# Kernel optimization log

Hardware: AMD Instinct MI355X
Metric: run time of the kernel (lower is better)

Reference implementation:

```python
import jax, jax.numpy as jnp
import numpy as np

EMB = 1024  # embedding_size in the torch module


def setup_inputs() -> dict:
    key = jax.random.key(0)
    ks = jax.random.split(key, 6)
    B, N, K = 64, 256, 4096
    y = jax.random.normal(ks[0], (B, N, 1024), dtype=jnp.float32)
    # nn.Linear weights, init normal(std=0.02), zero bias
    Wy_w = jax.random.normal(ks[1], (1024, 1024), dtype=jnp.float32) * 0.02  # [out,in]
    Wy_b = jnp.zeros((1024,), dtype=jnp.float32)
    Wz_w = jax.random.normal(ks[2], (1024, 2048), dtype=jnp.float32) * 0.02  # [out,in]
    Wz_b = jnp.zeros((1024,), dtype=jnp.float32)
    dic_z = jax.random.normal(ks[3], (K, 2048), dtype=jnp.float32)
    prior = jax.random.uniform(ks[4], (K,), dtype=jnp.float32)
    prior = prior / jnp.sum(prior)
    return {"y": y, "Wy_w": Wy_w, "Wy_b": Wy_b, "Wz_w": Wz_w, "Wz_b": Wz_b,
            "dic_z": dic_z, "prior": prior}


def reference(y, Wy_w, Wy_b, Wz_w, Wz_b, dic_z, prior):
    # h = Wy(y): [B,N,1024]; dz = Wz(dic_z): [K,1024]
    h = jnp.einsum('bni,oi->bno', y, Wy_w) + Wy_b
    dz = jnp.einsum('ki,oi->ko', dic_z, Wz_w) + Wz_b
    # attention over dictionary: [B,N,K]
    att = jax.nn.softmax(jnp.einsum('bnd,kd->bnk', h, dz) / jnp.sqrt(jnp.float32(EMB)), axis=-1)
    # z[b,n] = sum_k prior[k] * att[b,n,k] * dic_z[k]  -> [B,N,2048]
    # (avoids the [B,N,K,2048] intermediate the torch code materializes)
    z = jnp.einsum('bnk,k,ke->bne', att, prior, dic_z)
    return z
```

## Files before the change

kernel.cpp:

```cpp
#include <hip/hip_runtime.h>
#include <hip/hip_bf16.h>
#include <stdint.h>

typedef __bf16 bf16;
typedef __bf16 bf16x8 __attribute__((ext_vector_type(8)));
typedef float f32x4 __attribute__((ext_vector_type(4)));
typedef unsigned short ushort8 __attribute__((ext_vector_type(8)));

__device__ __forceinline__ void gload16(const bf16* g, char* l) {
  __builtin_amdgcn_global_load_lds(
      reinterpret_cast<const __attribute__((address_space(1))) unsigned int*>(
          reinterpret_cast<uintptr_t>(g)),
      reinterpret_cast<__attribute__((address_space(3))) unsigned int*>(
          reinterpret_cast<uintptr_t>(l)),
      16, 0, 0);
}

__global__ __launch_bounds__(256) void cast_bf16(const float* __restrict__ in,
                                                 bf16* __restrict__ out, int n8) {
  int i = blockIdx.x * blockDim.x + threadIdx.x;
  const int stride = gridDim.x * blockDim.x;
  for (; i < n8; i += stride) {
    const float4 v0 = reinterpret_cast<const float4*>(in)[i * 2];
    const float4 v1 = reinterpret_cast<const float4*>(in)[i * 2 + 1];
    bf16x8 o = { (bf16)v0.x, (bf16)v0.y, (bf16)v0.z, (bf16)v0.w,
                 (bf16)v1.x, (bf16)v1.y, (bf16)v1.z, (bf16)v1.w };
    reinterpret_cast<bf16x8*>(out)[i] = o;
  }
}

template <bool OUT_BF16, bool HAS_BIAS>
__global__ __launch_bounds__(256, 2) void gemm_occ(
    const bf16* __restrict__ A, const bf16* __restrict__ B,
    const float* __restrict__ bias, void* __restrict__ Cout,
    int M, int N, int K, float scale) {
  constexpr int BUFSZ = 32768;
  constexpr int BOFF = 16384;
  extern __shared__ char lds[];
  const int tid = threadIdx.x;
  const int lane = tid & 63, w = tid >> 6;

  const int gridN = N >> 7;
  const int nwg = gridDim.x;
  const int orig = blockIdx.x;
  int wgid;
  { const int q = nwg >> 3, r = nwg & 7, x = orig & 7, rest = orig >> 3;
    wgid = (x < r ? x * (q + 1) : r * (q + 1) + (x - r) * q) + rest; }
  const int m0 = (wgid / gridN) * 128;
  const int n0 = (wgid % gridN) * 128;

  const int srow = lane >> 3;
  const int scol = ((lane & 7) ^ srow) * 8;
  const bf16* gA = A + (size_t)(m0 + w * 32 + srow) * K + scol;
  const bf16* gB = B + (size_t)(n0 + w * 32 + srow) * K + scol;

  auto stage = [&](int t) {
    char* dst = lds + (size_t)(t & 1) * BUFSZ + (w * 32) * 128;
    const size_t kc = (size_t)t * 64;
#pragma unroll
    for (int i = 0; i < 4; ++i) {
      gload16(gA + (size_t)(i * 8) * K + kc, dst + i * 1024);
      gload16(gB + (size_t)(i * 8) * K + kc, dst + BOFF + i * 1024);
    }
  };

  const int fr = lane & 15, hi = lane >> 4;
  const int wm = w >> 1, wn = w & 1;
  const int abase = (wm * 64 + fr) * 128 + ((hi ^ (fr & 7)) << 4);
  const int bbase = BOFF + (wn * 64 + fr) * 128 + ((hi ^ (fr & 7)) << 4);

  f32x4 acc[4][4] = {};
  const int NT = K >> 6;

  stage(0);
  __syncthreads();

  for (int t = 0; t < NT; ++t) {
    const char* b = lds + (size_t)(t & 1) * BUFSZ;
    if (t + 1 < NT) stage(t + 1);
    bf16x8 a[4][2], bb[4][2];
#pragma unroll
    for (int mi = 0; mi < 4; ++mi) {
      a[mi][0] = *(const bf16x8*)(b + ((abase + mi * 2048)));
      a[mi][1] = *(const bf16x8*)(b + ((abase + mi * 2048) ^ 64));
    }
#pragma unroll
    for (int ni = 0; ni < 4; ++ni) {
      bb[ni][0] = *(const bf16x8*)(b + ((bbase + ni * 2048)));
      bb[ni][1] = *(const bf16x8*)(b + ((bbase + ni * 2048) ^ 64));
    }
#pragma unroll
    for (int mi = 0; mi < 4; ++mi)
#pragma unroll
      for (int ni = 0; ni < 4; ++ni) {
        acc[mi][ni] = __builtin_amdgcn_mfma_f32_16x16x32_bf16(a[mi][0], bb[ni][0], acc[mi][ni], 0, 0, 0);
        acc[mi][ni] = __builtin_amdgcn_mfma_f32_16x16x32_bf16(a[mi][1], bb[ni][1], acc[mi][ni], 0, 0, 0);
      }
    __syncthreads();
  }

  const int lro = hi * 4;
#pragma unroll
  for (int ni = 0; ni < 4; ++ni) {
    const int gcol = n0 + wn * 64 + ni * 16 + fr;
    float bvs = 0.f;
    if constexpr (HAS_BIAS) bvs = bias[gcol];
#pragma unroll
    for (int mi = 0; mi < 4; ++mi) {
      const int grow = m0 + wm * 64 + mi * 16 + lro;
#pragma unroll
      for (int j = 0; j < 4; ++j) {
        const float c = acc[mi][ni][j] * scale + bvs;
        if constexpr (OUT_BF16)
          ((bf16*)Cout)[(size_t)(grow + j) * N + gcol] = (bf16)c;
        else
          ((float*)Cout)[(size_t)(grow + j) * N + gcol] = c;
      }
    }
  }
}

__global__ __launch_bounds__(256) void prep_w3t(const float* __restrict__ dic,
                                                const float* __restrict__ prior,
                                                bf16* __restrict__ w3t) {
  const int KD = 4096, E = 2048;
  __shared__ bf16 t[64][72];
  const int k0 = blockIdx.x * 64, e0 = blockIdx.y * 64;
  const int tid = threadIdx.x;
  const int er = (tid & 15) * 4;
  const int kr = tid >> 4;
#pragma unroll
  for (int p = 0; p < 4; ++p) {
    const int k = kr + p * 16;
    const float pr = prior[k0 + k];
    const float4 v = *reinterpret_cast<const float4*>(dic + (size_t)(k0 + k) * E + e0 + er);
    t[er + 0][k] = (bf16)(v.x * pr);
    t[er + 1][k] = (bf16)(v.y * pr);
    t[er + 2][k] = (bf16)(v.z * pr);
    t[er + 3][k] = (bf16)(v.w * pr);
  }
  __syncthreads();
  const int e = tid >> 2, kc = (tid & 3) * 16;
  ushort8 a = *reinterpret_cast<ushort8*>(&t[e][kc]);
  ushort8 b = *reinterpret_cast<ushort8*>(&t[e][kc + 8]);
  unsigned short* dst = (unsigned short*)w3t + (size_t)(e0 + e) * KD + k0 + kc;
  *reinterpret_cast<ushort8*>(dst) = a;
  *reinterpret_cast<ushort8*>(dst + 8) = b;
}

__global__ __launch_bounds__(256) void softmax_rows(unsigned short* __restrict__ S) {
  const int K = 4096;
  unsigned short* row = S + (size_t)blockIdx.x * K;
  const int tid = threadIdx.x;
  const int lane = tid & 63, w = tid >> 6;
  __shared__ float red[8];

  ushort8 v0 = *reinterpret_cast<const ushort8*>(row + tid * 8);
  ushort8 v1 = *reinterpret_cast<const ushort8*>(row + 2048 + tid * 8);
  float x[16];
#pragma unroll
  for (int i = 0; i < 8; ++i) {
    x[i]     = __uint_as_float(((unsigned)v0[i]) << 16);
    x[8 + i] = __uint_as_float(((unsigned)v1[i]) << 16);
  }
  float mx = x[0];
#pragma unroll
  for (int i = 1; i < 16; ++i) mx = fmaxf(mx, x[i]);
#pragma unroll
  for (int o = 32; o; o >>= 1) mx = fmaxf(mx, __shfl_xor(mx, o));
  if (lane == 0) red[w] = mx;
  __syncthreads();
  mx = fmaxf(fmaxf(red[0], red[1]), fmaxf(red[2], red[3]));

  float s = 0.f;
#pragma unroll
  for (int i = 0; i < 16; ++i) { x[i] = __expf(x[i] - mx); s += x[i]; }
#pragma unroll
  for (int o = 32; o; o >>= 1) s += __shfl_xor(s, o);
  if (lane == 0) red[4 + w] = s;
  __syncthreads();
  const float inv = 1.f / (red[4] + red[5] + red[6] + red[7]);

  ushort8 o0, o1;
#pragma unroll
  for (int i = 0; i < 8; ++i) {
    bf16 b0 = (bf16)(x[i] * inv);
    bf16 b1 = (bf16)(x[8 + i] * inv);
    o0[i] = __builtin_bit_cast(unsigned short, b0);
    o1[i] = __builtin_bit_cast(unsigned short, b1);
  }
  *reinterpret_cast<ushort8*>(row + tid * 8) = o0;
  *reinterpret_cast<ushort8*>(row + 2048 + tid * 8) = o1;
}

extern "C" void kernel_launch(void* const* d_in, const int* in_sizes, int n_in,
                              void* d_out, int out_size, void* d_ws, size_t ws_size,
                              hipStream_t stream) {
  const float* y     = (const float*)d_in[0];
  const float* Wy_w  = (const float*)d_in[1];
  const float* Wy_b  = (const float*)d_in[2];
  const float* Wz_w  = (const float*)d_in[3];
  const float* Wz_b  = (const float*)d_in[4];
  const float* dic   = (const float*)d_in[5];
  const float* prior = (const float*)d_in[6];
  float* z = (float*)d_out;

  const int M = 16384, D = 1024, E = 2048, KD = 4096;
  const size_t LDSB = 65536;

  char* ws = (char*)d_ws;
  bf16* w3t  = (bf16*)(ws);
  bf16* h    = (bf16*)(ws + ((size_t)16 << 20));
  bf16* dzb  = (bf16*)(ws + ((size_t)48 << 20));
  bf16* S    = (bf16*)(ws + ((size_t)56 << 20));
  bf16* yb   = (bf16*)(ws + ((size_t)56 << 20));
  bf16* Wyb  = (bf16*)(ws + ((size_t)88 << 20));
  bf16* Wzb  = (bf16*)(ws + ((size_t)90 << 20));
  bf16* dicb = (bf16*)(ws + ((size_t)94 << 20));

  cast_bf16<<<2048, 256, 0, stream>>>(y, yb, M * D / 8);
  cast_bf16<<<512, 256, 0, stream>>>(Wy_w, Wyb, D * D / 8);
  cast_bf16<<<512, 256, 0, stream>>>(Wz_w, Wzb, D * E / 8);
  cast_bf16<<<1024, 256, 0, stream>>>(dic, dicb, KD * E / 8);
  prep_w3t<<<dim3(KD / 64, E / 64), 256, 0, stream>>>(dic, prior, w3t);
  gemm_occ<true, true><<<(M / 128) * (D / 128), 256, LDSB, stream>>>(
      yb, Wyb, Wy_b, h, M, D, D, 1.0f);
  gemm_occ<true, true><<<(KD / 128) * (D / 128), 256, LDSB, stream>>>(
      dicb, Wzb, Wz_b, dzb, KD, D, E, 1.0f);
  gemm_occ<true, false><<<(M / 128) * (KD / 128), 256, LDSB, stream>>>(
      h, dzb, nullptr, S, M, KD, D, 0.03125f);
  softmax_rows<<<M, 256, 0, stream>>>((unsigned short*)S);
  gemm_occ<false, false><<<(M / 128) * (E / 128), 256, LDSB, stream>>>(
      S, w3t, nullptr, z, M, E, KD, 1.0f);
}
```

Before: 578.8 us.

## Use 256x128 tiles with B fragments loaded directly from global into registers

```diff
diff --git a/kernel.cpp b/kernel.cpp
--- a/kernel.cpp
+++ b/kernel.cpp
@@ -30,74 +30,93 @@
 }
 
 template <bool OUT_BF16, bool HAS_BIAS>
-__global__ __launch_bounds__(256, 2) void gemm_occ(
+__global__ __launch_bounds__(256, 2) void gemm_bd(
     const bf16* __restrict__ A, const bf16* __restrict__ B,
     const float* __restrict__ bias, void* __restrict__ Cout,
     int M, int N, int K, float scale) {
   constexpr int BUFSZ = 32768;
-  constexpr int BOFF = 16384;
   extern __shared__ char lds[];
   const int tid = threadIdx.x;
   const int lane = tid & 63, w = tid >> 6;
 
-  const int gridN = N >> 7;
+  const int gridM = M >> 8;
   const int nwg = gridDim.x;
   const int orig = blockIdx.x;
   int wgid;
   { const int q = nwg >> 3, r = nwg & 7, x = orig & 7, rest = orig >> 3;
     wgid = (x < r ? x * (q + 1) : r * (q + 1) + (x - r) * q) + rest; }
-  const int m0 = (wgid / gridN) * 128;
-  const int n0 = (wgid % gridN) * 128;
+  const int m0 = (wgid % gridM) * 256;
+  const int n0 = (wgid / gridM) * 128;
 
   const int srow = lane >> 3;
   const int scol = ((lane & 7) ^ srow) * 8;
-  const bf16* gA = A + (size_t)(m0 + w * 32 + srow) * K + scol;
-  const bf16* gB = B + (size_t)(n0 + w * 32 + srow) * K + scol;
-
-  auto stage = [&](int t) {
-    char* dst = lds + (size_t)(t & 1) * BUFSZ + (w * 32) * 128;
+  const bf16* gA = A + (size_t)(m0 + w * 64 + srow) * K + scol;
+
+  auto stageA = [&](int t) {
+    char* dst = lds + (size_t)(t & 1) * BUFSZ + (w * 64) * 128;
     const size_t kc = (size_t)t * 64;
 #pragma unroll
-    for (int i = 0; i < 4; ++i) {
+    for (int i = 0; i < 8; ++i)
       gload16(gA + (size_t)(i * 8) * K + kc, dst + i * 1024);
-      gload16(gB + (size_t)(i * 8) * K + kc, dst + BOFF + i * 1024);
-    }
   };
 
   const int fr = lane & 15, hi = lane >> 4;
   const int wm = w >> 1, wn = w & 1;
-  const int abase = (wm * 64 + fr) * 128 + ((hi ^ (fr & 7)) << 4);
-  const int bbase = BOFF + (wn * 64 + fr) * 128 + ((hi ^ (fr & 7)) << 4);
-
-  f32x4 acc[4][4] = {};
+  const int abase = (wm * 128 + fr) * 128 + ((hi ^ (fr & 7)) << 4);
+
+  const bf16* gB[4];
+#pragma unroll
+  for (int ni = 0; ni < 4; ++ni)
+    gB[ni] = B + (size_t)(n0 + wn * 64 + ni * 16 + fr) * K + hi * 8;
+
+  f32x4 acc[8][4] = {};
   const int NT = K >> 6;
 
-  stage(0);
-  __syncthreads();
-
-  for (int t = 0; t < NT; ++t) {
-    const char* b = lds + (size_t)(t & 1) * BUFSZ;
-    if (t + 1 < NT) stage(t + 1);
-    bf16x8 a[4][2], bb[4][2];
-#pragma unroll
-    for (int mi = 0; mi < 4; ++mi) {
-      a[mi][0] = *(const bf16x8*)(b + ((abase + mi * 2048)));
-      a[mi][1] = *(const bf16x8*)(b + ((abase + mi * 2048) ^ 64));
-    }
-#pragma unroll
-    for (int ni = 0; ni < 4; ++ni) {
-      bb[ni][0] = *(const bf16x8*)(b + ((bbase + ni * 2048)));
-      bb[ni][1] = *(const bf16x8*)(b + ((bbase + ni * 2048) ^ 64));
-    }
-#pragma unroll
-    for (int mi = 0; mi < 4; ++mi)
-#pragma unroll
-      for (int ni = 0; ni < 4; ++ni) {
-        acc[mi][ni] = __builtin_amdgcn_mfma_f32_16x16x32_bf16(a[mi][0], bb[ni][0], acc[mi][ni], 0, 0, 0);
-        acc[mi][ni] = __builtin_amdgcn_mfma_f32_16x16x32_bf16(a[mi][1], bb[ni][1], acc[mi][ni], 0, 0, 0);
-      }
-    __syncthreads();
-  }
+  bf16x8 bA[4][2], bB[4][2];
+#define LOADB(DST, T) do {                                                     \
+    _Pragma("unroll") for (int ni = 0; ni < 4; ++ni) {                         \
+      DST[ni][0] = *(const bf16x8*)(gB[ni] + (size_t)(T) * 64);                \
+      DST[ni][1] = *(const bf16x8*)(gB[ni] + (size_t)(T) * 64 + 32);           \
+    } } while (0)
+
+  stageA(0);
+  LOADB(bA, 0);
+  __syncthreads();
+
+#define MFMA_(a0, a1, bc, accv)                                                \
+    accv = __builtin_amdgcn_mfma_f32_16x16x32_bf16(a0, bc[0], accv, 0, 0, 0); \
+    accv = __builtin_amdgcn_mfma_f32_16x16x32_bf16(a1, bc[1], accv, 0, 0, 0);
+
+#define ITER(T, BC, BN) do {                                                   \
+    const char* bp = lds + (size_t)((T) & 1) * BUFSZ;                          \
+    if ((T) + 1 < NT) { stageA((T) + 1); LOADB(BN, (T) + 1); }                 \
+    bf16x8 a[4][2];                                                            \
+    _Pragma("unroll") for (int mi = 0; mi < 4; ++mi) {                         \
+      a[mi][0] = *(const bf16x8*)(bp + (abase + mi * 2048));                   \
+      a[mi][1] = *(const bf16x8*)(bp + ((abase + mi * 2048) ^ 64));            \
+    }                                                                          \
+    _Pragma("unroll") for (int mi = 0; mi < 4; ++mi)                           \
+      _Pragma("unroll") for (int ni = 0; ni < 4; ++ni) {                       \
+        MFMA_(a[mi][0], a[mi][1], BC[ni], acc[mi][ni]);                        \
+      }                                                                        \
+    _Pragma("unroll") for (int mi = 0; mi < 4; ++mi) {                         \
+      a[mi][0] = *(const bf16x8*)(bp + (abase + (4 + mi) * 2048));             \
+      a[mi][1] = *(const bf16x8*)(bp + ((abase + (4 + mi) * 2048) ^ 64));      \
+    }                                                                          \
+    _Pragma("unroll") for (int mi = 0; mi < 4; ++mi)                           \
+      _Pragma("unroll") for (int ni = 0; ni < 4; ++ni) {                       \
+        MFMA_(a[mi][0], a[mi][1], BC[ni], acc[4 + mi][ni]);                    \
+      }                                                                        \
+    __syncthreads();                                                           \
+  } while (0)
+
+  for (int t = 0; t < NT; t += 2) {
+    ITER(t, bA, bB);
+    ITER(t + 1, bB, bA);
+  }
+#undef ITER
+#undef MFMA_
+#undef LOADB
 
   const int lro = hi * 4;
 #pragma unroll
@@ -106,8 +125,8 @@
     float bvs = 0.f;
     if constexpr (HAS_BIAS) bvs = bias[gcol];
 #pragma unroll
-    for (int mi = 0; mi < 4; ++mi) {
-      const int grow = m0 + wm * 64 + mi * 16 + lro;
+    for (int mi = 0; mi < 8; ++mi) {
+      const int grow = m0 + wm * 128 + mi * 16 + lro;
 #pragma unroll
       for (int j = 0; j < 4; ++j) {
         const float c = acc[mi][ni][j] * scale + bvs;
@@ -223,13 +242,13 @@
   cast_bf16<<<512, 256, 0, stream>>>(Wz_w, Wzb, D * E / 8);
   cast_bf16<<<1024, 256, 0, stream>>>(dic, dicb, KD * E / 8);
   prep_w3t<<<dim3(KD / 64, E / 64), 256, 0, stream>>>(dic, prior, w3t);
-  gemm_occ<true, true><<<(M / 128) * (D / 128), 256, LDSB, stream>>>(
+  gemm_bd<true, true><<<(M / 256) * (D / 128), 256, LDSB, stream>>>(
       yb, Wyb, Wy_b, h, M, D, D, 1.0f);
-  gemm_occ<true, true><<<(KD / 128) * (D / 128), 256, LDSB, stream>>>(
+  gemm_bd<true, true><<<(KD / 256) * (D / 128), 256, LDSB, stream>>>(
       dicb, Wzb, Wz_b, dzb, KD, D, E, 1.0f);
-  gemm_occ<true, false><<<(M / 128) * (KD / 128), 256, LDSB, stream>>>(
+  gemm_bd<true, false><<<(M / 256) * (KD / 128), 256, LDSB, stream>>>(
       h, dzb, nullptr, S, M, KD, D, 0.03125f);
   softmax_rows<<<M, 256, 0, stream>>>((unsigned short*)S);
-  gemm_occ<false, false><<<(M / 128) * (E / 128), 256, LDSB, stream>>>(
+  gemm_bd<false, false><<<(M / 256) * (E / 128), 256, LDSB, stream>>>(
       S, w3t, nullptr, z, M, E, KD, 1.0f);
 }
```

New measurement: 803.0 us. 38.7% more time.

## Switch GEMMs to 32x32x16 MFMA with fragment-ordered LDS layout; fuse dic cast

Applied to the files above, without the earlier changes.

```diff
diff --git a/kernel.cpp b/kernel.cpp
--- a/kernel.cpp
+++ b/kernel.cpp
@@ -3,8 +3,9 @@
 #include <stdint.h>
 
 typedef __bf16 bf16;
+typedef __bf16 bf16x4 __attribute__((ext_vector_type(4)));
 typedef __bf16 bf16x8 __attribute__((ext_vector_type(8)));
-typedef float f32x4 __attribute__((ext_vector_type(4)));
+typedef float f32x16 __attribute__((ext_vector_type(16)));
 typedef unsigned short ushort8 __attribute__((ext_vector_type(8)));
 
 __device__ __forceinline__ void gload16(const bf16* g, char* l) {
@@ -30,7 +31,7 @@
 }
 
 template <bool OUT_BF16, bool HAS_BIAS>
-__global__ __launch_bounds__(256, 2) void gemm_occ(
+__global__ __launch_bounds__(256, 2) void gemm32(
     const bf16* __restrict__ A, const bf16* __restrict__ B,
     const float* __restrict__ bias, void* __restrict__ Cout,
     int M, int N, int K, float scale) {
@@ -49,27 +50,25 @@
   const int m0 = (wgid / gridN) * 128;
   const int n0 = (wgid % gridN) * 128;
 
-  const int srow = lane >> 3;
-  const int scol = ((lane & 7) ^ srow) * 8;
-  const bf16* gA = A + (size_t)(m0 + w * 32 + srow) * K + scol;
-  const bf16* gB = B + (size_t)(n0 + w * 32 + srow) * K + scol;
+  const int frow = lane & 31;
+  const int fkh  = lane >> 5;
+  const bf16* gA = A + (size_t)(m0 + w * 32 + frow) * K + fkh * 8;
+  const bf16* gB = B + (size_t)(n0 + w * 32 + frow) * K + fkh * 8;
 
   auto stage = [&](int t) {
-    char* dst = lds + (size_t)(t & 1) * BUFSZ + (w * 32) * 128;
+    char* dst = lds + (size_t)(t & 1) * BUFSZ + w * 4096;
     const size_t kc = (size_t)t * 64;
 #pragma unroll
-    for (int i = 0; i < 4; ++i) {
-      gload16(gA + (size_t)(i * 8) * K + kc, dst + i * 1024);
-      gload16(gB + (size_t)(i * 8) * K + kc, dst + BOFF + i * 1024);
+    for (int ks = 0; ks < 4; ++ks) {
+      gload16(gA + kc + ks * 16, dst + ks * 1024);
+      gload16(gB + kc + ks * 16, dst + BOFF + ks * 1024);
     }
   };
 
-  const int fr = lane & 15, hi = lane >> 4;
   const int wm = w >> 1, wn = w & 1;
-  const int abase = (wm * 64 + fr) * 128 + ((hi ^ (fr & 7)) << 4);
-  const int bbase = BOFF + (wn * 64 + fr) * 128 + ((hi ^ (fr & 7)) << 4);
-
-  f32x4 acc[4][4] = {};
+  const int lofs = lane * 16;
+
+  f32x16 acc[2][2] = {};
   const int NT = K >> 6;
 
   stage(0);
@@ -78,50 +77,52 @@
   for (int t = 0; t < NT; ++t) {
     const char* b = lds + (size_t)(t & 1) * BUFSZ;
     if (t + 1 < NT) stage(t + 1);
-    bf16x8 a[4][2], bb[4][2];
-#pragma unroll
-    for (int mi = 0; mi < 4; ++mi) {
-      a[mi][0] = *(const bf16x8*)(b + ((abase + mi * 2048)));
-      a[mi][1] = *(const bf16x8*)(b + ((abase + mi * 2048) ^ 64));
-    }
-#pragma unroll
-    for (int ni = 0; ni < 4; ++ni) {
-      bb[ni][0] = *(const bf16x8*)(b + ((bbase + ni * 2048)));
-      bb[ni][1] = *(const bf16x8*)(b + ((bbase + ni * 2048) ^ 64));
-    }
-#pragma unroll
-    for (int mi = 0; mi < 4; ++mi)
-#pragma unroll
-      for (int ni = 0; ni < 4; ++ni) {
-        acc[mi][ni] = __builtin_amdgcn_mfma_f32_16x16x32_bf16(a[mi][0], bb[ni][0], acc[mi][ni], 0, 0, 0);
-        acc[mi][ni] = __builtin_amdgcn_mfma_f32_16x16x32_bf16(a[mi][1], bb[ni][1], acc[mi][ni], 0, 0, 0);
-      }
+    bf16x8 a[2][4], bb[2][4];
+#pragma unroll
+    for (int ti = 0; ti < 2; ++ti)
+#pragma unroll
+      for (int ks = 0; ks < 4; ++ks)
+        a[ti][ks] = *(const bf16x8*)(b + ((wm * 2 + ti) * 4 + ks) * 1024 + lofs);
+#pragma unroll
+    for (int ni = 0; ni < 2; ++ni)
+#pragma unroll
+      for (int ks = 0; ks < 4; ++ks)
+        bb[ni][ks] = *(const bf16x8*)(b + BOFF + ((wn * 2 + ni) * 4 + ks) * 1024 + lofs);
+#pragma unroll
+    for (int ks = 0; ks < 4; ++ks)
+#pragma unroll
+      for (int ti = 0; ti < 2; ++ti)
+#pragma unroll
+        for (int ni = 0; ni < 2; ++ni)
+          acc[ti][ni] = __builtin_amdgcn_mfma_f32_32x32x16_bf16(
+              a[ti][ks], bb[ni][ks], acc[ti][ni], 0, 0, 0);
     __syncthreads();
   }
 
-  const int lro = hi * 4;
-#pragma unroll
-  for (int ni = 0; ni < 4; ++ni) {
-    const int gcol = n0 + wn * 64 + ni * 16 + fr;
+#pragma unroll
+  for (int ni = 0; ni < 2; ++ni) {
+    const int gcol = n0 + wn * 64 + ni * 32 + frow;
     float bvs = 0.f;
     if constexpr (HAS_BIAS) bvs = bias[gcol];
 #pragma unroll
-    for (int mi = 0; mi < 4; ++mi) {
-      const int grow = m0 + wm * 64 + mi * 16 + lro;
-#pragma unroll
-      for (int j = 0; j < 4; ++j) {
-        const float c = acc[mi][ni][j] * scale + bvs;
+    for (int ti = 0; ti < 2; ++ti) {
+      const int rowb = m0 + wm * 64 + ti * 32 + 4 * fkh;
+#pragma unroll
+      for (int r = 0; r < 16; ++r) {
+        const int grow = rowb + (r & 3) + 8 * (r >> 2);
+        const float c = acc[ti][ni][r] * scale + bvs;
         if constexpr (OUT_BF16)
-          ((bf16*)Cout)[(size_t)(grow + j) * N + gcol] = (bf16)c;
+          ((bf16*)Cout)[(size_t)grow * N + gcol] = (bf16)c;
         else
-          ((float*)Cout)[(size_t)(grow + j) * N + gcol] = c;
+          ((float*)Cout)[(size_t)grow * N + gcol] = c;
       }
     }
   }
 }
 
-__global__ __launch_bounds__(256) void prep_w3t(const float* __restrict__ dic,
+__global__ __launch_bounds__(256) void prep_dic(const float* __restrict__ dic,
                                                 const float* __restrict__ prior,
+                                                bf16* __restrict__ dicb,
                                                 bf16* __restrict__ w3t) {
   const int KD = 4096, E = 2048;
   __shared__ bf16 t[64][72];
@@ -134,6 +135,8 @@
     const int k = kr + p * 16;
     const float pr = prior[k0 + k];
     const float4 v = *reinterpret_cast<const float4*>(dic + (size_t)(k0 + k) * E + e0 + er);
+    bf16x4 db = { (bf16)v.x, (bf16)v.y, (bf16)v.z, (bf16)v.w };
+    *reinterpret_cast<bf16x4*>(dicb + (size_t)(k0 + k) * E + e0 + er) = db;
     t[er + 0][k] = (bf16)(v.x * pr);
     t[er + 1][k] = (bf16)(v.y * pr);
     t[er + 2][k] = (bf16)(v.z * pr);
@@ -221,15 +224,14 @@
   cast_bf16<<<2048, 256, 0, stream>>>(y, yb, M * D / 8);
   cast_bf16<<<512, 256, 0, stream>>>(Wy_w, Wyb, D * D / 8);
   cast_bf16<<<512, 256, 0, stream>>>(Wz_w, Wzb, D * E / 8);
-  cast_bf16<<<1024, 256, 0, stream>>>(dic, dicb, KD * E / 8);
-  prep_w3t<<<dim3(KD / 64, E / 64), 256, 0, stream>>>(dic, prior, w3t);
-  gemm_occ<true, true><<<(M / 128) * (D / 128), 256, LDSB, stream>>>(
+  prep_dic<<<dim3(KD / 64, E / 64), 256, 0, stream>>>(dic, prior, dicb, w3t);
+  gemm32<true, true><<<(M / 128) * (D / 128), 256, LDSB, stream>>>(
       yb, Wyb, Wy_b, h, M, D, D, 1.0f);
-  gemm_occ<true, true><<<(KD / 128) * (D / 128), 256, LDSB, stream>>>(
+  gemm32<true, true><<<(KD / 128) * (D / 128), 256, LDSB, stream>>>(
       dicb, Wzb, Wz_b, dzb, KD, D, E, 1.0f);
-  gemm_occ<true, false><<<(M / 128) * (KD / 128), 256, LDSB, stream>>>(
+  gemm32<true, false><<<(M / 128) * (KD / 128), 256, LDSB, stream>>>(
       h, dzb, nullptr, S, M, KD, D, 0.03125f);
   softmax_rows<<<M, 256, 0, stream>>>((unsigned short*)S);
-  gemm_occ<false, false><<<(M / 128) * (E / 128), 256, LDSB, stream>>>(
+  gemm32<false, false><<<(M / 128) * (E / 128), 256, LDSB, stream>>>(
       S, w3t, nullptr, z, M, E, KD, 1.0f);
 }
```

After: 1.022 ms. +76.6%, slower.
